# Optimization experiments

Measured on AMD Instinct MI355X. Metric: run time of the kernel, lower is better.

## Reference

```python
import jax, jax.numpy as jnp
import numpy as np

N_NODES = 100_000
N_EDGES = 1_000_000
IN_FTS = 64
EDGE_IN_FTS = 64
OUT_DIM = 64
LN_EPS = 1e-5


def setup_inputs() -> dict:
    key = jax.random.key(0)
    ks = jax.random.split(key, 9)
    def lin(k, fan_in, fan_out):
        bound = 1.0 / np.sqrt(fan_in)
        kw, kb = jax.random.split(k)
        W = jax.random.uniform(kw, (fan_out, fan_in), jnp.float32, -bound, bound)
        b = jax.random.uniform(kb, (fan_out,), jnp.float32, -bound, bound)
        return W, b
    node_fts = jax.random.normal(ks[0], (N_NODES, IN_FTS), jnp.float32)
    edge_fts = jax.random.normal(ks[1], (N_EDGES, EDGE_IN_FTS), jnp.float32)
    edges = jax.random.randint(ks[2], (2, N_EDGES), 0, N_NODES, jnp.int64)
    W_init, b_init = lin(ks[3], EDGE_IN_FTS, OUT_DIM)
    W_mlp, b_mlp = lin(ks[4], 2 * IN_FTS + OUT_DIM, OUT_DIM)
    W_alpha, b_alpha = lin(ks[5], 2 * IN_FTS + OUT_DIM, 1)
    return {
        "node_fts": node_fts, "edge_fts": edge_fts, "edges": edges,
        "W_init": W_init, "b_init": b_init,
        "W_mlp": W_mlp, "b_mlp": b_mlp,
        "W_alpha": W_alpha, "b_alpha": b_alpha,
    }


def _layer_norm(x):
    # F.layer_norm over last dim, no affine params
    m = jnp.mean(x, axis=-1, keepdims=True)
    v = jnp.mean(jnp.square(x - m), axis=-1, keepdims=True)
    return (x - m) * jax.lax.rsqrt(v + LN_EPS)


def reference(node_fts, edge_fts, edges, W_init, b_init, W_mlp, b_mlp, W_alpha, b_alpha):
    # initial edge projection: [E, edge_in] -> [E, out_dim]
    e = edge_fts @ W_init.T + b_init
    # gather head/tail node features: [E, in_fts] each
    head_vectors = jnp.take(node_fts, edges[0], axis=0)
    tail_vectors = jnp.take(node_fts, edges[1], axis=0)
    combined = jnp.concatenate([e, head_vectors, tail_vectors], axis=1)  # [E, 2*in+out]
    alpha = jax.nn.sigmoid(combined @ W_alpha.T + b_alpha)  # [E, 1]
    processed = jnp.tanh(combined @ W_mlp.T + b_mlp)        # [E, out_dim]
    right_side = _layer_norm(processed) * alpha
    return _layer_norm(e + right_side)
```

## Files before the change

kernel.cpp:

```cpp
#include <hip/hip_runtime.h>
#include <hip/hip_bf16.h>

typedef __bf16 bf16;
typedef bf16 bf16x8 __attribute__((ext_vector_type(8)));
typedef float f32x4 __attribute__((ext_vector_type(4)));

#define MFMA16(a, b, c) __builtin_amdgcn_mfma_f32_16x16x32_bf16((a), (b), (c), 0, 0, 0)
#define UNROLL _Pragma("unroll")

__device__ __forceinline__ float fast_rcp(float x) { return __builtin_amdgcn_rcpf(x); }
__device__ __forceinline__ float fast_rsq(float x) { return __builtin_amdgcn_rsqf(x); }
__device__ __forceinline__ float fast_tanh(float x) {
    float e = __expf(2.0f * x);
    return 1.0f - 2.0f * fast_rcp(e + 1.0f);
}
__device__ __forceinline__ float fast_sigmoid(float x) {
    return fast_rcp(1.0f + __expf(-x));
}

__device__ __forceinline__ f32x4 ldnt4(const float* __restrict__ p) {
    return __builtin_nontemporal_load((const f32x4*)p);
}

__device__ __forceinline__ bf16x8 cvt8(const float* __restrict__ p) {
    f32x4 a = *(const f32x4*)p;
    f32x4 b = *(const f32x4*)(p + 4);
    bf16x8 r;
    r[0] = (bf16)a[0]; r[1] = (bf16)a[1]; r[2] = (bf16)a[2]; r[3] = (bf16)a[3];
    r[4] = (bf16)b[0]; r[5] = (bf16)b[1]; r[6] = (bf16)b[2]; r[7] = (bf16)b[3];
    return r;
}
__device__ __forceinline__ bf16x8 cvt8v(f32x4 a, f32x4 b) {
    bf16x8 r;
    r[0] = (bf16)a[0]; r[1] = (bf16)a[1]; r[2] = (bf16)a[2]; r[3] = (bf16)a[3];
    r[4] = (bf16)b[0]; r[5] = (bf16)b[1]; r[6] = (bf16)b[2]; r[7] = (bf16)b[3];
    return r;
}

template <int CTRL>
__device__ __forceinline__ float dpp_add(float v) {
    int t = __builtin_amdgcn_update_dpp(0, __float_as_int(v), CTRL, 0xF, 0xF, false);
    return v + __int_as_float(t);
}
__device__ __forceinline__ float sum16(float v) {
    v = dpp_add<0x121>(v);
    v = dpp_add<0x122>(v);
    v = dpp_add<0x124>(v);
    v = dpp_add<0x128>(v);
    return v;
}

#define WS_WAF  8192
#define WS_BMF  8320
#define WS_BAF  8576

__global__ void prep_kernel(const float* __restrict__ W_init,
                            const float* __restrict__ b_init,
                            const float* __restrict__ W_mlp,
                            const float* __restrict__ b_mlp,
                            const float* __restrict__ W_alpha,
                            const float* __restrict__ b_alpha,
                            const float* __restrict__ node_fts,
                            char* __restrict__ ws,
                            bf16* __restrict__ ncache,
                            int nchunks)
{
    const int idx = blockIdx.x * 256 + threadIdx.x;
    if (blockIdx.x < 17) {
        bf16*  Wf  = (bf16*)ws;
        bf16*  waf = (bf16*)(ws + WS_WAF);
        float* bMf = (float*)(ws + WS_BMF);
        float* bAf = (float*)(ws + WS_BAF);
        if (idx < 4096) {
            const int o = idx >> 6, k = idx & 63;
            float acc = 0.f;
            for (int j = 0; j < 64; ++j)
                acc += W_mlp[o * 192 + j] * W_init[j * 64 + k];
            Wf[o * 64 + k] = (bf16)acc;
        } else if (idx < 4160) {
            const int o = idx - 4096;
            float acc = b_mlp[o];
            for (int j = 0; j < 64; ++j)
                acc += W_mlp[o * 192 + j] * b_init[j];
            bMf[o] = acc;
        } else if (idx < 4224) {
            const int k = idx - 4160;
            float acc = 0.f;
            for (int j = 0; j < 64; ++j)
                acc += W_alpha[j] * W_init[j * 64 + k];
            waf[k] = (bf16)acc;
        } else if (idx == 4224) {
            float acc = b_alpha[0];
            for (int j = 0; j < 64; ++j)
                acc += W_alpha[j] * b_init[j];
            bAf[0] = acc;
        }
    } else {
        const int i = idx - 17 * 256;
        if (i < nchunks) {
            f32x4 a = ldnt4(node_fts + (size_t)i * 8);
            f32x4 b = ldnt4(node_fts + (size_t)i * 8 + 4);
            *(bf16x8*)(ncache + (size_t)i * 8) = cvt8v(a, b);
        }
    }
}

template <bool NB>
__global__ __launch_bounds__(256, 3)
void edge_update_kernel(const float* __restrict__ node_fts,
                        const float* __restrict__ edge_fts,
                        const int*   __restrict__ edges,
                        const float* __restrict__ W_init,
                        const float* __restrict__ b_init,
                        const float* __restrict__ W_mlp,
                        const float* __restrict__ W_alpha,
                        const char*  __restrict__ ws,
                        const bf16*  __restrict__ nc,
                        float* __restrict__ out,
                        int E, int g0, int g1)
{
    __shared__ bf16 sW2[64][200];
    __shared__ bf16 sWa[224];

    const int tid  = threadIdx.x;
    const int lane = tid & 63;
    const int wv   = tid >> 6;
    const int n    = lane & 15;
    const int q    = lane >> 4;

    const bf16*  Wf  = (const bf16*)ws;
    const bf16*  waf = (const bf16*)(ws + WS_WAF);
    const float* bMf = (const float*)(ws + WS_BMF);
    const float* bAf = (const float*)(ws + WS_BAF);

    for (int c = tid; c < 64 * 24; c += 256) {
        const int r = c / 24;
        const int o = (c - r * 24) * 8;
        if (o < 64) *(bf16x8*)(&sW2[r][o]) = *(const bf16x8*)(Wf + r * 64 + o);
        else        *(bf16x8*)(&sW2[r][o]) = cvt8(W_mlp + r * 192 + o);
    }
    if (tid < 24) {
        const int o = tid * 8;
        if (o < 64) *(bf16x8*)(&sWa[o]) = *(const bf16x8*)(waf + o);
        else        *(bf16x8*)(&sWa[o]) = cvt8(W_alpha + o);
    }
    __syncthreads();

    bf16x8 B1[2][4];
    UNROLL
    for (int kk = 0; kk < 2; ++kk)
        UNROLL
        for (int t = 0; t < 4; ++t)
            B1[kk][t] = cvt8(W_init + (t * 16 + n) * 64 + kk * 32 + q * 8);

    float bI[4], bM[4];
    UNROLL
    for (int t = 0; t < 4; ++t) {
        bI[t] = b_init[t * 16 + n];
        bM[t] = bMf[t * 16 + n];
    }
    const float bA = bAf[0];

    for (int g = g0 + blockIdx.x * 4 + wv; g < g1; g += gridDim.x * 4) {
        const int e0 = g << 4;
        const int h  = edges[e0 + n];
        const int tl = edges[E + e0 + n];

        bf16x8 A[6];
        const float* ep = edge_fts + (size_t)(e0 + n) * 64;
        A[0] = cvt8v(ldnt4(ep + q * 8), ldnt4(ep + q * 8 + 4));
        A[1] = cvt8v(ldnt4(ep + 32 + q * 8), ldnt4(ep + 32 + q * 8 + 4));
        if constexpr (NB) {
            const bf16* hp = nc + (size_t)h * 64;
            const bf16* tp = nc + (size_t)tl * 64;
            A[2] = *(const bf16x8*)(hp + q * 8);
            A[3] = *(const bf16x8*)(hp + 32 + q * 8);
            A[4] = *(const bf16x8*)(tp + q * 8);
            A[5] = *(const bf16x8*)(tp + 32 + q * 8);
        } else {
            const float* hp = node_fts + (size_t)h * 64;
            const float* tp = node_fts + (size_t)tl * 64;
            A[2] = cvt8(hp + q * 8);
            A[3] = cvt8(hp + 32 + q * 8);
            A[4] = cvt8(tp + q * 8);
            A[5] = cvt8(tp + 32 + q * 8);
        }

        f32x4 accE[4] = { f32x4{0,0,0,0}, f32x4{0,0,0,0}, f32x4{0,0,0,0}, f32x4{0,0,0,0} };
        UNROLL
        for (int kk = 0; kk < 2; ++kk)
            UNROLL
            for (int t = 0; t < 4; ++t) accE[t] = MFMA16(A[kk], B1[kk][t], accE[t]);

        f32x4 accP[4] = { f32x4{0,0,0,0}, f32x4{0,0,0,0}, f32x4{0,0,0,0}, f32x4{0,0,0,0} };
        f32x4 accA = f32x4{0,0,0,0};
        UNROLL
        for (int kk = 0; kk < 6; ++kk) {
            accA = MFMA16(A[kk], *(const bf16x8*)(&sWa[kk * 32 + q * 8]), accA);
            UNROLL
            for (int t = 0; t < 4; ++t)
                accP[t] = MFMA16(A[kk], *(const bf16x8*)(&sW2[t * 16 + n][kk * 32 + q * 8]), accP[t]);
        }

        float eF[4][4], pv[4][4], alpha[4];
        UNROLL
        for (int t = 0; t < 4; ++t)
            UNROLL
            for (int r = 0; r < 4; ++r) eF[t][r] = accE[t][r] + bI[t];
        UNROLL
        for (int r = 0; r < 4; ++r) alpha[r] = fast_sigmoid(accA[r] + bA);
        UNROLL
        for (int t = 0; t < 4; ++t)
            UNROLL
            for (int r = 0; r < 4; ++r) pv[t][r] = fast_tanh(accP[t][r] + bM[t]);

        float s1[4], s2[4];
        UNROLL
        for (int r = 0; r < 4; ++r) {
            s1[r] = pv[0][r] + pv[1][r] + pv[2][r] + pv[3][r];
            s2[r] = pv[0][r]*pv[0][r] + pv[1][r]*pv[1][r] + pv[2][r]*pv[2][r] + pv[3][r]*pv[3][r];
        }
        UNROLL
        for (int r = 0; r < 4; ++r) { s1[r] = sum16(s1[r]); s2[r] = sum16(s2[r]); }

        float o2[4][4];
        UNROLL
        for (int r = 0; r < 4; ++r) {
            const float mean = s1[r] * 0.015625f;
            const float var  = fmaxf(s2[r] * 0.015625f - mean * mean, 0.0f);
            const float rs   = fast_rsq(var + 1e-5f);
            UNROLL
            for (int t = 0; t < 4; ++t)
                o2[t][r] = eF[t][r] + (pv[t][r] - mean) * rs * alpha[r];
        }

        UNROLL
        for (int r = 0; r < 4; ++r) {
            s1[r] = o2[0][r] + o2[1][r] + o2[2][r] + o2[3][r];
            s2[r] = o2[0][r]*o2[0][r] + o2[1][r]*o2[1][r] + o2[2][r]*o2[2][r] + o2[3][r]*o2[3][r];
        }
        UNROLL
        for (int r = 0; r < 4; ++r) { s1[r] = sum16(s1[r]); s2[r] = sum16(s2[r]); }

        UNROLL
        for (int r = 0; r < 4; ++r) {
            const float mean = s1[r] * 0.015625f;
            const float var  = fmaxf(s2[r] * 0.015625f - mean * mean, 0.0f);
            const float rs   = fast_rsq(var + 1e-5f);
            UNROLL
            for (int t = 0; t < 4; ++t)
                out[((size_t)e0 + q * 4 + r) * 64 + t * 16 + n] = (o2[t][r] - mean) * rs;
        }
    }
}

extern "C" void kernel_launch(void* const* d_in, const int* in_sizes, int n_in,
                              void* d_out, int out_size, void* d_ws, size_t ws_size,
                              hipStream_t stream) {
    const float* node_fts = (const float*)d_in[0];
    const float* edge_fts = (const float*)d_in[1];
    const int*   edges    = (const int*)d_in[2];
    const float* W_init   = (const float*)d_in[3];
    const float* b_init   = (const float*)d_in[4];
    const float* W_mlp    = (const float*)d_in[5];
    const float* b_mlp    = (const float*)d_in[6];
    const float* W_alpha  = (const float*)d_in[7];
    const float* b_alpha  = (const float*)d_in[8];
    float* out = (float*)d_out;
    char*  ws  = (char*)d_ws;

    const int E = in_sizes[2] / 2;
    const int N = in_sizes[0] / 64;
    const int totalGroups = E >> 4;

    int cacheRows = ((N + 1) / 2 + 15) & ~15;
    cacheRows += (E - cacheRows) & 15;
    const bool useCache = (E >= cacheRows + 16) && (cacheRows > 0);

    bf16* ncache = useCache ? (bf16*)(out + (size_t)(E - cacheRows) * 64) : (bf16*)nullptr;
    const int nchunks = useCache ? N * 8 : 0;

    const int prep_blocks = 17 + (nchunks + 255) / 256;
    hipLaunchKernelGGL(prep_kernel, dim3(prep_blocks), dim3(256), 0, stream,
                       W_init, b_init, W_mlp, b_mlp, W_alpha, b_alpha,
                       node_fts, ws, ncache, nchunks);

    if (useCache) {
        const int mainGroups = (E - cacheRows) >> 4;
        hipLaunchKernelGGL((edge_update_kernel<true>), dim3(2048), dim3(256), 0, stream,
                           node_fts, edge_fts, edges, W_init, b_init,
                           W_mlp, W_alpha, ws, ncache, out, E, 0, mainGroups);
        hipLaunchKernelGGL((edge_update_kernel<false>), dim3(256), dim3(256), 0, stream,
                           node_fts, edge_fts, edges, W_init, b_init,
                           W_mlp, W_alpha, ws, (const bf16*)nullptr, out, E,
                           mainGroups, totalGroups);
    } else {
        hipLaunchKernelGGL((edge_update_kernel<false>), dim3(2048), dim3(256), 0, stream,
                           node_fts, edge_fts, edges, W_init, b_init,
                           W_mlp, W_alpha, ws, (const bf16*)nullptr, out, E,
                           0, totalGroups);
    }
}
```

Baseline: 703.4 us.

## Software-pipeline edge loads and stage output through LDS for coalesced stores

Each wave now prefetches the next group's edge features and gathered node rows into registers while computing the current group, and loads the edge indices two groups ahead. Results are written to a per-wave LDS buffer and then stored as contiguous nontemporal float4 writes instead of strided scalar stores. Index loads become nontemporal, and the fallback tail kernel launches 2048 blocks instead of 256. This hides gather latency and improves write coalescing, at the cost of more registers and 16KB of extra LDS per block, which may reduce occupancy.

Result: slower. 734.3 us (+4.4%).

```diff
diff --git a/kernel.cpp b/kernel.cpp
--- a/kernel.cpp
+++ b/kernel.cpp
@@ -20,6 +20,12 @@
 
 __device__ __forceinline__ f32x4 ldnt4(const float* __restrict__ p) {
     return __builtin_nontemporal_load((const f32x4*)p);
+}
+__device__ __forceinline__ int ldnti(const int* __restrict__ p) {
+    return __builtin_nontemporal_load(p);
+}
+__device__ __forceinline__ void stnt4(float* __restrict__ p, f32x4 v) {
+    __builtin_nontemporal_store(v, (f32x4*)p);
 }
 
 __device__ __forceinline__ bf16x8 cvt8(const float* __restrict__ p) {
@@ -105,6 +111,34 @@
     }
 }
 
+#define ISSUE_STAGE(gs, hh, tt)                                               \
+    {                                                                         \
+        const float* ep_ = edge_fts + (((size_t)(gs) << 4) + n) * 64;         \
+        efS0 = ldnt4(ep_ + q * 8);                                            \
+        efS1 = ldnt4(ep_ + q * 8 + 4);                                        \
+        efS2 = ldnt4(ep_ + 32 + q * 8);                                       \
+        efS3 = ldnt4(ep_ + 32 + q * 8 + 4);                                   \
+        if constexpr (NB) {                                                   \
+            const bf16* hp_ = nc + (size_t)(hh) * 64;                         \
+            const bf16* tp_ = nc + (size_t)(tt) * 64;                         \
+            nhS0 = *(const bf16x8*)(hp_ + q * 8);                             \
+            nhS1 = *(const bf16x8*)(hp_ + 32 + q * 8);                        \
+            ntS0 = *(const bf16x8*)(tp_ + q * 8);                             \
+            ntS1 = *(const bf16x8*)(tp_ + 32 + q * 8);                        \
+        } else {                                                              \
+            const float* hp_ = node_fts + (size_t)(hh) * 64;                  \
+            const float* tp_ = node_fts + (size_t)(tt) * 64;                  \
+            nhF0 = *(const f32x4*)(hp_ + q * 8);                              \
+            nhF1 = *(const f32x4*)(hp_ + q * 8 + 4);                          \
+            nhF2 = *(const f32x4*)(hp_ + 32 + q * 8);                         \
+            nhF3 = *(const f32x4*)(hp_ + 32 + q * 8 + 4);                     \
+            ntF0 = *(const f32x4*)(tp_ + q * 8);                              \
+            ntF1 = *(const f32x4*)(tp_ + q * 8 + 4);                          \
+            ntF2 = *(const f32x4*)(tp_ + 32 + q * 8);                         \
+            ntF3 = *(const f32x4*)(tp_ + 32 + q * 8 + 4);                     \
+        }                                                                     \
+    }
+
 template <bool NB>
 __global__ __launch_bounds__(256, 3)
 void edge_update_kernel(const float* __restrict__ node_fts,
@@ -119,8 +153,9 @@
                         float* __restrict__ out,
                         int E, int g0, int g1)
 {
-    __shared__ bf16 sW2[64][200];
-    __shared__ bf16 sWa[224];
+    __shared__ bf16  sW2[64][200];
+    __shared__ bf16  sWa[224];
+    __shared__ float sOut[4][1024];
 
     const int tid  = threadIdx.x;
     const int lane = tid & 63;
@@ -161,29 +196,45 @@
     }
     const float bA = bAf[0];
 
-    for (int g = g0 + blockIdx.x * 4 + wv; g < g1; g += gridDim.x * 4) {
-        const int e0 = g << 4;
-        const int h  = edges[e0 + n];
-        const int tl = edges[E + e0 + n];
-
+    const int gStep = gridDim.x * 4;
+    int g = g0 + blockIdx.x * 4 + wv;
+    if (g >= g1) return;
+
+    f32x4  efS0, efS1, efS2, efS3;
+    bf16x8 nhS0, nhS1, ntS0, ntS1;
+    f32x4  nhF0, nhF1, nhF2, nhF3, ntF0, ntF1, ntF2, ntF3;
+
+    {
+        const int h0 = ldnti(edges + ((size_t)g << 4) + n);
+        const int t0 = ldnti(edges + E + ((size_t)g << 4) + n);
+        ISSUE_STAGE(g, h0, t0);
+    }
+    int gl = (g + gStep < g1) ? g + gStep : g;
+    int hn = ldnti(edges + ((size_t)gl << 4) + n);
+    int tn = ldnti(edges + E + ((size_t)gl << 4) + n);
+
+    float* const ob = &sOut[wv][0];
+
+    for (;;) {
         bf16x8 A[6];
-        const float* ep = edge_fts + (size_t)(e0 + n) * 64;
-        A[0] = cvt8v(ldnt4(ep + q * 8), ldnt4(ep + q * 8 + 4));
-        A[1] = cvt8v(ldnt4(ep + 32 + q * 8), ldnt4(ep + 32 + q * 8 + 4));
+        A[0] = cvt8v(efS0, efS1);
+        A[1] = cvt8v(efS2, efS3);
         if constexpr (NB) {
-            const bf16* hp = nc + (size_t)h * 64;
-            const bf16* tp = nc + (size_t)tl * 64;
-            A[2] = *(const bf16x8*)(hp + q * 8);
-            A[3] = *(const bf16x8*)(hp + 32 + q * 8);
-            A[4] = *(const bf16x8*)(tp + q * 8);
-            A[5] = *(const bf16x8*)(tp + 32 + q * 8);
+            A[2] = nhS0; A[3] = nhS1;
+            A[4] = ntS0; A[5] = ntS1;
         } else {
-            const float* hp = node_fts + (size_t)h * 64;
-            const float* tp = node_fts + (size_t)tl * 64;
-            A[2] = cvt8(hp + q * 8);
-            A[3] = cvt8(hp + 32 + q * 8);
-            A[4] = cvt8(tp + q * 8);
-            A[5] = cvt8(tp + 32 + q * 8);
+            A[2] = cvt8v(nhF0, nhF1); A[3] = cvt8v(nhF2, nhF3);
+            A[4] = cvt8v(ntF0, ntF1); A[5] = cvt8v(ntF2, ntF3);
+        }
+
+        const bool haveNext = (g + gStep) < g1;
+        const int  gs = haveNext ? g + gStep : g;
+        ISSUE_STAGE(gs, hn, tn);
+        {
+            const int g2  = gs + gStep;
+            const int g2l = (g2 < g1) ? g2 : gs;
+            hn = ldnti(edges + ((size_t)g2l << 4) + n);
+            tn = ldnti(edges + E + ((size_t)g2l << 4) + n);
         }
 
         f32x4 accE[4] = { f32x4{0,0,0,0}, f32x4{0,0,0,0}, f32x4{0,0,0,0}, f32x4{0,0,0,0} };
@@ -249,8 +300,17 @@
             const float rs   = fast_rsq(var + 1e-5f);
             UNROLL
             for (int t = 0; t < 4; ++t)
-                out[((size_t)e0 + q * 4 + r) * 64 + t * 16 + n] = (o2[t][r] - mean) * rs;
-        }
+                ob[(q * 4 + r) * 64 + t * 16 + n] = (o2[t][r] - mean) * rs;
+        }
+        {
+            float* op = out + (((size_t)g << 4)) * 64;
+            UNROLL
+            for (int j = 0; j < 4; ++j)
+                stnt4(op + j * 256 + lane * 4, *(const f32x4*)(ob + j * 256 + lane * 4));
+        }
+
+        if (!haveNext) return;
+        g += gStep;
     }
 }
 
@@ -290,7 +350,7 @@
         hipLaunchKernelGGL((edge_update_kernel<true>), dim3(2048), dim3(256), 0, stream,
                            node_fts, edge_fts, edges, W_init, b_init,
                            W_mlp, W_alpha, ws, ncache, out, E, 0, mainGroups);
-        hipLaunchKernelGGL((edge_update_kernel<false>), dim3(256), dim3(256), 0, stream,
+        hipLaunchKernelGGL((edge_update_kernel<false>), dim3(2048), dim3(256), 0, stream,
                            node_fts, edge_fts, edges, W_init, b_init,
                            W_mlp, W_alpha, ws, (const bf16*)nullptr, out, E,
                            mainGroups, totalGroups);
```
